# Performance work log

Hardware: AMD Instinct MI355X
Metric: run time of the kernel (lower is better)

The kernel has to match this reference:

```python
import jax, jax.numpy as jnp
import numpy as np

EPS = 1e-8

@jax.custom_vjp
def spike(x):
    # Heaviside forward, SuperSpike surrogate gradient in backward
    return (x > 0.0).astype(x.dtype)

def _spike_fwd(x):
    return spike(x), x

def _spike_bwd(x, g):
    return (g / (1.0 + 10.0 * jnp.abs(x)) ** 2,)

spike.defvjp(_spike_fwd, _spike_bwd)


def setup_inputs() -> dict:
    key = jax.random.key(0)
    k1, k2, k3, k4 = jax.random.split(key, 4)
    B, T, I, O = 128, 128, 1024, 1024
    x = jax.random.normal(k1, (B, T, I), dtype=jnp.float32)
    # w ~ N(0, 1/sqrt(I)) per reset_parameters
    w = jax.random.normal(k2, (I, O), dtype=jnp.float32) * np.float32(1.0 / np.sqrt(I))
    # beta ~ N(0.7, 0.01), clamped to [0,1]
    beta = jnp.clip(0.7 + 0.01 * jax.random.normal(k3, (1,), dtype=jnp.float32), 0.0, 1.0)
    # b ~ N(1.0, 0.01), clamped to >= 0
    b = jnp.clip(1.0 + 0.01 * jax.random.normal(k4, (1024,), dtype=jnp.float32), 0.0, None)
    return {"x": x, "w": w, "beta": beta, "b": b}


def reference(x, w, beta, b):
    # x: [B, T, I]; w: [I, O]; beta: [1]; b: [O]
    h = jnp.einsum('btc,cd->btd', x, w)                 # [B, T, O]
    d = jnp.einsum('ab,ac->bc', w, w)                    # lateral reset matrix [O, O]
    norm = (w ** 2).sum(0)                               # [O]
    inv_norm = 1.0 / (norm + EPS)
    B, O = x.shape[0], w.shape[1]

    def step(carry, h_t):
        mem, spk = carry
        rst = spk @ d                                    # [B, O]
        mem = (mem - rst) * beta + h_t * (1.0 - beta)
        mthr = mem * inv_norm - b
        spk = spike(mthr)
        return (mem, spk), spk

    init = (jnp.zeros((B, O), x.dtype), jnp.zeros((B, O), x.dtype))
    _, spk_rec = jax.lax.scan(step, init, jnp.swapaxes(h, 0, 1))  # [T, B, O]
    spk_rec = jnp.swapaxes(spk_rec, 0, 1)                # [B, T, O]
    loss = 0.5 * (spk_rec ** 2).mean()
    return spk_rec, loss
```

## Files before the change

### kernel.cpp

```cpp
#include <hip/hip_runtime.h>
#include <hip/hip_fp16.h>

#define B_ 128
#define T_ 128
#define I_ 1024
#define O_ 1024
#define M_ (B_*T_)
#define NOUT (M_*O_)

typedef __attribute__((ext_vector_type(8))) _Float16 half8;
typedef __attribute__((ext_vector_type(4))) float floatx4;

__device__ __forceinline__ void gld_lds16(const void* g, void* l) {
    __builtin_amdgcn_global_load_lds((const __attribute__((address_space(1))) void*)g,
                                     (__attribute__((address_space(3))) void*)l,
                                     16, 0, 0);
}

__device__ __forceinline__ void barrier_lds_only() {
    asm volatile("" ::: "memory");
    __builtin_amdgcn_s_waitcnt(0xC07F);
    __builtin_amdgcn_s_barrier();
    asm volatile("" ::: "memory");
}

__device__ __forceinline__ void split3h(float x, unsigned short& h,
                                        unsigned short& m, unsigned short& l) {
    __half f0 = __float2half(x);
    float r1 = x - __half2float(f0);
    __half f1 = __float2half(r1);
    float r2 = r1 - __half2float(f1);
    __half f2 = __float2half(r2);
    h = __half_as_ushort(f0);
    m = __half_as_ushort(f1);
    l = __half_as_ushort(f2);
}

__global__ __launch_bounds__(256) void split_x(const float* __restrict__ X,
                                               unsigned short* __restrict__ Xh,
                                               unsigned short* __restrict__ Xm,
                                               unsigned short* __restrict__ Xl) {
    size_t base = ((size_t)blockIdx.x * 256 + threadIdx.x) * 4;
    float4 v = *(const float4*)(X + base);
    ushort4 hh, mm, ll;
    split3h(v.x, hh.x, mm.x, ll.x);
    split3h(v.y, hh.y, mm.y, ll.y);
    split3h(v.z, hh.z, mm.z, ll.z);
    split3h(v.w, hh.w, mm.w, ll.w);
    *(ushort4*)(Xh + base) = hh;
    *(ushort4*)(Xm + base) = mm;
    *(ushort4*)(Xl + base) = ll;
}

__global__ __launch_bounds__(256) void split_wt(const float* __restrict__ W,
                                                unsigned short* __restrict__ WTh,
                                                unsigned short* __restrict__ WTm,
                                                unsigned short* __restrict__ WTl) {
    __shared__ float t[64][65];
    const int tid = threadIdx.x;
    const int tx = tid & 63, ty4 = tid >> 6;
    const int r0 = blockIdx.x * 64, c0 = blockIdx.y * 64;
#pragma unroll
    for (int j = 0; j < 16; ++j) {
        int row = j * 4 + ty4;
        t[row][tx] = W[(size_t)(r0 + row) * O_ + c0 + tx];
    }
    __syncthreads();
#pragma unroll
    for (int j = 0; j < 16; ++j) {
        int i = j * 4 + ty4;
        float v = t[tx][i];
        unsigned short h, m, l;
        split3h(v, h, m, l);
        size_t off = (size_t)(c0 + i) * I_ + r0 + tx;
        WTh[off] = h; WTm[off] = m; WTl[off] = l;
    }
}

__global__ __launch_bounds__(256, 3) void gemm_h_mfma(
        const unsigned short* __restrict__ Xh, const unsigned short* __restrict__ Xm,
        const unsigned short* __restrict__ Xl, const unsigned short* __restrict__ WTh,
        const unsigned short* __restrict__ WTm, const unsigned short* __restrict__ WTl,
        float* __restrict__ H) {
    const int K = I_, N = O_;
    __shared__ unsigned short P[6][128 * 32];

    const int tid = threadIdx.x;
    const int lane = tid & 63;
    const int wid = tid >> 6;
    const int wrow = wid >> 1, wcol = wid & 1;
    const int l15 = lane & 15, quad = lane >> 4;
    const int bm = blockIdx.x * 128, bn = blockIdx.y * 128;

    const int srow = tid >> 2, sch = tid & 3;
    const int schg = sch ^ ((srow >> 1) & 3);
    const unsigned short* gsrc[6];
    gsrc[0] = Xh  + (size_t)(bm + srow) * K + schg * 8;
    gsrc[1] = Xm  + (size_t)(bm + srow) * K + schg * 8;
    gsrc[2] = Xl  + (size_t)(bm + srow) * K + schg * 8;
    gsrc[3] = WTh + (size_t)(bn + srow) * K + schg * 8;
    gsrc[4] = WTm + (size_t)(bn + srow) * K + schg * 8;
    gsrc[5] = WTl + (size_t)(bn + srow) * K + schg * 8;

    floatx4 acc[4][4];
#pragma unroll
    for (int mt = 0; mt < 4; ++mt)
#pragma unroll
        for (int nt = 0; nt < 4; ++nt) acc[mt][nt] = (floatx4)(0.f);

    for (int kt = 0; kt < 32; ++kt) {
        const int k0 = kt * 32;
        __syncthreads();
#pragma unroll
        for (int p = 0; p < 6; ++p) {
            unsigned short* dst = (unsigned short*)P + p * 4096 + tid * 8;
            gld_lds16(gsrc[p] + k0, dst);
            gld_lds16(gsrc[p] + (size_t)64 * K + k0, dst + 2048);
        }
        __syncthreads();

        half8 Af[3][4];
#pragma unroll
        for (int pa = 0; pa < 3; ++pa)
#pragma unroll
            for (int mt = 0; mt < 4; ++mt) {
                int row = wrow * 64 + mt * 16 + l15;
                int chk = quad ^ ((row >> 1) & 3);
                Af[pa][mt] = *(const half8*)((const unsigned short*)P + pa * 4096 + row * 32 + chk * 8);
            }
#pragma unroll
        for (int pb = 0; pb < 3; ++pb) {
            half8 Bf[4];
#pragma unroll
            for (int nt = 0; nt < 4; ++nt) {
                int col = wcol * 64 + nt * 16 + l15;
                int chk = quad ^ ((col >> 1) & 3);
                Bf[nt] = *(const half8*)((const unsigned short*)P + (3 + pb) * 4096 + col * 32 + chk * 8);
            }
#pragma unroll
            for (int nt = 0; nt < 4; ++nt)
#pragma unroll
                for (int mt = 0; mt < 4; ++mt) {
                    acc[mt][nt] = __builtin_amdgcn_mfma_f32_16x16x32_f16(Af[0][mt], Bf[nt], acc[mt][nt], 0, 0, 0);
                    if (pb < 2)
                        acc[mt][nt] = __builtin_amdgcn_mfma_f32_16x16x32_f16(Af[1][mt], Bf[nt], acc[mt][nt], 0, 0, 0);
                    if (pb == 0)
                        acc[mt][nt] = __builtin_amdgcn_mfma_f32_16x16x32_f16(Af[2][mt], Bf[nt], acc[mt][nt], 0, 0, 0);
                }
        }
    }

#pragma unroll
    for (int mt = 0; mt < 4; ++mt)
#pragma unroll
        for (int nt = 0; nt < 4; ++nt) {
            int grow = bm + wrow * 64 + mt * 16 + quad * 4;
            int gcol = bn + wcol * 64 + nt * 16 + l15;
            float* hp = H + (size_t)grow * N + gcol;
#pragma unroll
            for (int r = 0; r < 4; ++r) hp[(size_t)r * N] = acc[mt][nt][r];
        }
}

__global__ __launch_bounds__(256) void gemm_wtw(const float* __restrict__ W,
                                                float* __restrict__ D) {
    const int K = I_, N = O_;
    __shared__ float As[32][68];
    __shared__ float Bs[32][68];
    const int tid = threadIdx.x;
    const int tx = tid & 15, ty = tid >> 4;
    const int bj = blockIdx.x * 64, bo = blockIdx.y * 64;
    const int lr = tid >> 4;
    const int lc = (tid & 15) << 2;

    float acc[4][4];
#pragma unroll
    for (int m = 0; m < 4; m++)
#pragma unroll
        for (int n = 0; n < 4; n++) acc[m][n] = 0.f;

    for (int k0 = 0; k0 < K; k0 += 32) {
        float4 a0 = *(const float4*)(W + (size_t)(k0 + lr) * N + bj + lc);
        float4 a1 = *(const float4*)(W + (size_t)(k0 + lr + 16) * N + bj + lc);
        float4 b0 = *(const float4*)(W + (size_t)(k0 + lr) * N + bo + lc);
        float4 b1 = *(const float4*)(W + (size_t)(k0 + lr + 16) * N + bo + lc);
        __syncthreads();
        *(float4*)&As[lr][lc] = a0; *(float4*)&As[lr + 16][lc] = a1;
        *(float4*)&Bs[lr][lc] = b0; *(float4*)&Bs[lr + 16][lc] = b1;
        __syncthreads();
#pragma unroll
        for (int k = 0; k < 32; ++k) {
            float4 av = *(const float4*)&As[k][ty * 4];
            float4 bv = *(const float4*)&Bs[k][tx * 4];
            float am[4] = {av.x, av.y, av.z, av.w};
            float bb[4] = {bv.x, bv.y, bv.z, bv.w};
#pragma unroll
            for (int m = 0; m < 4; m++)
#pragma unroll
                for (int n = 0; n < 4; n++) acc[m][n] += am[m] * bb[n];
        }
    }
#pragma unroll
    for (int m = 0; m < 4; m++) {
        float4 v = make_float4(acc[m][0], acc[m][1], acc[m][2], acc[m][3]);
        *(float4*)(D + (size_t)(bj + ty * 4 + m) * N + bo + tx * 4) = v;
    }
}

__global__ void colnorm_diag(const float* __restrict__ D, float* __restrict__ invn,
                             unsigned int* __restrict__ counter) {
    int o = blockIdx.x * 256 + threadIdx.x;
    if (o == 0) *counter = 0u;
    invn[o] = 1.0f / (D[(size_t)o * O_ + o] + 1e-8f);
}

__global__ __launch_bounds__(256) void scan_kernel(const float* __restrict__ h,
                                                   const float* __restrict__ d,
                                                   const float* __restrict__ invn,
                                                   const float* __restrict__ bias,
                                                   const float* __restrict__ beta,
                                                   float* __restrict__ out,
                                                   unsigned int* __restrict__ spike_count) {
    __shared__ int lst[2][O_];
    __shared__ int cnt[T_ + 1];
    __shared__ unsigned int red[256];

    const int tid = threadIdx.x;
    const int lane = tid & 63;
    const int b = blockIdx.x;
    const int o4 = tid * 4;
    const float betav = beta[0];
    const float omb = 1.0f - betav;

    const float4 invn4 = *(const float4*)(invn + o4);
    const float4 b4 = *(const float4*)(bias + o4);
    float4 mem4 = make_float4(0.f, 0.f, 0.f, 0.f);

    for (int i = tid; i <= T_; i += 256) cnt[i] = 0;
    unsigned int local_count = 0;
    const float* hb = h + (size_t)b * T_ * O_;
    float* ob = out + (size_t)b * T_ * O_;
    const unsigned long long below = (lane == 63) ? 0xFFFFFFFFFFFFFFFFull >> 1
                                                  : ((1ull << lane) - 1ull);

    float4 hcur = *(const float4*)(hb + o4);
    __syncthreads();

    for (int t = 0; t < T_; ++t) {
        const int p = t & 1, q = p ^ 1;
        const int n = cnt[t];

        float4 hnext = make_float4(0.f, 0.f, 0.f, 0.f);
        if (t + 1 < T_) hnext = *(const float4*)(hb + (size_t)(t + 1) * O_ + o4);

        float4 rst = make_float4(0.f, 0.f, 0.f, 0.f);
        int i = 0;
        for (; i + 16 <= n; i += 16) {
            float4 v[16];
#pragma unroll
            for (int u = 0; u < 16; ++u) {
                const int j = lst[p][i + u];
                v[u] = *(const float4*)(d + (size_t)j * O_ + o4);
            }
#pragma unroll
            for (int u = 0; u < 16; ++u) {
                rst.x += v[u].x; rst.y += v[u].y;
                rst.z += v[u].z; rst.w += v[u].w;
            }
        }
        for (; i + 4 <= n; i += 4) {
            float4 v[4];
#pragma unroll
            for (int u = 0; u < 4; ++u) {
                const int j = lst[p][i + u];
                v[u] = *(const float4*)(d + (size_t)j * O_ + o4);
            }
#pragma unroll
            for (int u = 0; u < 4; ++u) {
                rst.x += v[u].x; rst.y += v[u].y;
                rst.z += v[u].z; rst.w += v[u].w;
            }
        }
        for (; i < n; ++i) {
            const int j = lst[p][i];
            float4 v = *(const float4*)(d + (size_t)j * O_ + o4);
            rst.x += v.x; rst.y += v.y; rst.z += v.z; rst.w += v.w;
        }

        mem4.x = (mem4.x - rst.x) * betav + hcur.x * omb;
        mem4.y = (mem4.y - rst.y) * betav + hcur.y * omb;
        mem4.z = (mem4.z - rst.z) * betav + hcur.z * omb;
        mem4.w = (mem4.w - rst.w) * betav + hcur.w * omb;

        const int s[4] = {(mem4.x * invn4.x - b4.x) > 0.0f,
                          (mem4.y * invn4.y - b4.y) > 0.0f,
                          (mem4.z * invn4.z - b4.z) > 0.0f,
                          (mem4.w * invn4.w - b4.w) > 0.0f};

        float4 sv = make_float4(s[0] ? 1.f : 0.f, s[1] ? 1.f : 0.f,
                                s[2] ? 1.f : 0.f, s[3] ? 1.f : 0.f);
        *(float4*)(ob + (size_t)t * O_ + o4) = sv;
        local_count += (unsigned)(s[0] + s[1] + s[2] + s[3]);

        unsigned long long mk0 = __ballot(s[0]);
        unsigned long long mk1 = __ballot(s[1]);
        unsigned long long mk2 = __ballot(s[2]);
        unsigned long long mk3 = __ballot(s[3]);
        const int c0 = __popcll(mk0), c1 = __popcll(mk1), c2 = __popcll(mk2);
        const int tot = c0 + c1 + c2 + __popcll(mk3);
        int base = 0;
        if (lane == 0 && tot) base = atomicAdd(&cnt[t + 1], tot);
        base = __shfl(base, 0, 64);
        if (s[0]) lst[q][base + __popcll(mk0 & below)] = o4 + 0;
        base += c0;
        if (s[1]) lst[q][base + __popcll(mk1 & below)] = o4 + 1;
        base += c1;
        if (s[2]) lst[q][base + __popcll(mk2 & below)] = o4 + 2;
        base += c2;
        if (s[3]) lst[q][base + __popcll(mk3 & below)] = o4 + 3;

        barrier_lds_only();
        hcur = hnext;
    }

    red[tid] = local_count;
    __syncthreads();
    for (int st = 128; st > 0; st >>= 1) {
        if (tid < st) red[tid] += red[tid + st];
        __syncthreads();
    }
    if (tid == 0) atomicAdd(spike_count, red[0]);
}

__global__ void finalize_loss(const unsigned int* __restrict__ spike_count,
                              float* __restrict__ loss_out) {
    *loss_out = 0.5f * ((float)(*spike_count) / 16777216.0f);
}

extern "C" void kernel_launch(void* const* d_in, const int* in_sizes, int n_in,
                              void* d_out, int out_size, void* d_ws, size_t ws_size,
                              hipStream_t stream) {
    const float* x    = (const float*)d_in[0];
    const float* w    = (const float*)d_in[1];
    const float* beta = (const float*)d_in[2];
    const float* bias = (const float*)d_in[3];
    float* out = (float*)d_out;

    char* ws = (char*)d_ws;
    float* h    = (float*)ws;
    float* dmat = (float*)(ws + (size_t)67108864);
    float* invn = (float*)(ws + (size_t)71303168);
    unsigned int* cntp = (unsigned int*)(ws + (size_t)71307264);
    unsigned short* wt_h = (unsigned short*)(ws + (size_t)71311360);
    unsigned short* wt_m = (unsigned short*)(ws + (size_t)73408512);
    unsigned short* wt_l = (unsigned short*)(ws + (size_t)75505664);
    unsigned short* x_h  = (unsigned short*)(ws + (size_t)77602816);
    unsigned short* x_m  = (unsigned short*)(ws + (size_t)111157248);
    unsigned short* x_l  = (unsigned short*)(ws + (size_t)144711680);

    split_x<<<M_ * I_ / 1024, 256, 0, stream>>>(x, x_h, x_m, x_l);
    split_wt<<<dim3(I_ / 64, O_ / 64), 256, 0, stream>>>(w, wt_h, wt_m, wt_l);
    gemm_h_mfma<<<dim3(M_ / 128, O_ / 128), 256, 0, stream>>>(x_h, x_m, x_l,
                                                              wt_h, wt_m, wt_l, h);
    gemm_wtw<<<dim3(O_ / 64, O_ / 64), 256, 0, stream>>>(w, dmat);
    colnorm_diag<<<O_ / 256, 256, 0, stream>>>(dmat, invn, cntp);
    scan_kernel<<<B_, 256, 0, stream>>>(h, dmat, invn, bias, beta, out, cntp);
    finalize_loss<<<1, 1, 0, stream>>>(cntp, out + (size_t)NOUT);
}
```

Baseline: 489.0 us.

## Double-buffer LDS and widen GEMM tile to 128x256 with 512 threads

The split-fp16 GEMM that computes h now uses 512-thread blocks over a 128x256 output tile, so each A tile feeds twice as many columns. It also double-buffers LDS and issues global-to-LDS loads for the next K step while the current one is computed, replacing the two-barrier load-then-compute loop. This aims to hide global load latency and cut A-operand traffic, at the cost of about 144KB of LDS per block and lower occupancy. The epilogue (not shown) must match the new wcol/bn mapping, and the waitcnt immediate and single-barrier scheme must fully order the buffer reuse.

```diff
diff --git a/kernel.cpp b/kernel.cpp
--- a/kernel.cpp
+++ b/kernel.cpp
@@ -77,30 +77,46 @@
     }
 }
 
-__global__ __launch_bounds__(256, 3) void gemm_h_mfma(
+__global__ __launch_bounds__(512, 2) void gemm_h_mfma(
         const unsigned short* __restrict__ Xh, const unsigned short* __restrict__ Xm,
         const unsigned short* __restrict__ Xl, const unsigned short* __restrict__ WTh,
         const unsigned short* __restrict__ WTm, const unsigned short* __restrict__ WTl,
         float* __restrict__ H) {
     const int K = I_, N = O_;
-    __shared__ unsigned short P[6][128 * 32];
+    __shared__ unsigned short P[2][36864];
 
     const int tid = threadIdx.x;
     const int lane = tid & 63;
     const int wid = tid >> 6;
-    const int wrow = wid >> 1, wcol = wid & 1;
+    const int wrow = wid >> 2;
+    const int wcol = wid & 3;
     const int l15 = lane & 15, quad = lane >> 4;
-    const int bm = blockIdx.x * 128, bn = blockIdx.y * 128;
+    const int bm = blockIdx.x * 128, bn = blockIdx.y * 256;
 
     const int srow = tid >> 2, sch = tid & 3;
     const int schg = sch ^ ((srow >> 1) & 3);
-    const unsigned short* gsrc[6];
-    gsrc[0] = Xh  + (size_t)(bm + srow) * K + schg * 8;
-    gsrc[1] = Xm  + (size_t)(bm + srow) * K + schg * 8;
-    gsrc[2] = Xl  + (size_t)(bm + srow) * K + schg * 8;
-    gsrc[3] = WTh + (size_t)(bn + srow) * K + schg * 8;
-    gsrc[4] = WTm + (size_t)(bn + srow) * K + schg * 8;
-    gsrc[5] = WTl + (size_t)(bn + srow) * K + schg * 8;
+    const unsigned short* gsrcA[3];
+    const unsigned short* gsrcB[3];
+    gsrcA[0] = Xh  + (size_t)(bm + srow) * K + schg * 8;
+    gsrcA[1] = Xm  + (size_t)(bm + srow) * K + schg * 8;
+    gsrcA[2] = Xl  + (size_t)(bm + srow) * K + schg * 8;
+    gsrcB[0] = WTh + (size_t)(bn + srow) * K + schg * 8;
+    gsrcB[1] = WTm + (size_t)(bn + srow) * K + schg * 8;
+    gsrcB[2] = WTl + (size_t)(bn + srow) * K + schg * 8;
+
+    auto stage = [&](int kt) {
+        unsigned short* wb = &P[0][0] + (size_t)(kt & 1) * 36864;
+        const size_t k0 = (size_t)kt * 32;
+#pragma unroll
+        for (int p = 0; p < 3; ++p)
+            gld_lds16(gsrcA[p] + k0, wb + p * 4096 + tid * 8);
+#pragma unroll
+        for (int p = 0; p < 3; ++p) {
+            unsigned short* bb = wb + 12288 + p * 8192 + tid * 8;
+            gld_lds16(gsrcB[p] + k0, bb);
+            gld_lds16(gsrcB[p] + (size_t)128 * K + k0, bb + 4096);
+        }
+    };
 
     floatx4 acc[4][4];
 #pragma unroll
@@ -108,34 +124,36 @@
 #pragma unroll
         for (int nt = 0; nt < 4; ++nt) acc[mt][nt] = (floatx4)(0.f);
 
+    stage(0);
+
     for (int kt = 0; kt < 32; ++kt) {
-        const int k0 = kt * 32;
-        __syncthreads();
-#pragma unroll
-        for (int p = 0; p < 6; ++p) {
-            unsigned short* dst = (unsigned short*)P + p * 4096 + tid * 8;
-            gld_lds16(gsrc[p] + k0, dst);
-            gld_lds16(gsrc[p] + (size_t)64 * K + k0, dst + 2048);
-        }
-        __syncthreads();
+        const unsigned short* rb = &P[0][0] + (size_t)(kt & 1) * 36864;
+
+        asm volatile("" ::: "memory");
+        __builtin_amdgcn_s_waitcnt(0x1F70);
+        __builtin_amdgcn_s_barrier();
+        asm volatile("" ::: "memory");
 
         half8 Af[3][4];
 #pragma unroll
         for (int pa = 0; pa < 3; ++pa)
 #pragma unroll
             for (int mt = 0; mt < 4; ++mt) {
-                int row = wrow * 64 + mt * 16 + l15;
-                int chk = quad ^ ((row >> 1) & 3);
-                Af[pa][mt] = *(const half8*)((const unsigned short*)P + pa * 4096 + row * 32 + chk * 8);
-            }
+                const int row = wrow * 64 + mt * 16 + l15;
+                const int chk = quad ^ ((row >> 1) & 3);
+                Af[pa][mt] = *(const half8*)(rb + pa * 4096 + row * 32 + chk * 8);
+            }
+
+        if (kt < 31) stage(kt + 1);
+
 #pragma unroll
         for (int pb = 0; pb < 3; ++pb) {
             half8 Bf[4];
 #pragma unroll
             for (int nt = 0; nt < 4; ++nt) {
-                int col = wcol * 64 + nt * 16 + l15;
-                int chk = quad ^ ((col >> 1) & 3);
-                Bf[nt] = *(const half8*)((const unsigned short*)P + (3 + pb) * 4096 + col * 32 + chk * 8);
+                const int col = wcol * 64 + nt * 16 + l15;
+                const int chk = quad ^ ((col >> 1) & 3);
+                Bf[nt] = *(const half8*)(rb + 12288 + pb * 8192 + col * 32 + chk * 8);
             }
 #pragma unroll
             for (int nt = 0; nt < 4; ++nt)
@@ -360,7 +378,7 @@
 
     split_x<<<M_ * I_ / 1024, 256, 0, stream>>>(x, x_h, x_m, x_l);
     split_wt<<<dim3(I_ / 64, O_ / 64), 256, 0, stream>>>(w, wt_h, wt_m, wt_l);
-    gemm_h_mfma<<<dim3(M_ / 128, O_ / 128), 256, 0, stream>>>(x_h, x_m, x_l,
+    gemm_h_mfma<<<dim3(M_ / 128, O_ / 256), 512, 0, stream>>>(x_h, x_m, x_l,
                                                               wt_h, wt_m, wt_l, h);
     gemm_wtw<<<dim3(O_ / 64, O_ / 64), 256, 0, stream>>>(w, dmat);
     colnorm_diag<<<O_ / 256, 256, 0, stream>>>(dmat, invn, cntp);
```

Measured after the change: 456.3 us. -6.7%, faster.
